# Optimization experiments

Measured on AMD Instinct MI355X. Metric: run time of the kernel, lower is better.

The kernel has to match this reference:

```python
import jax, jax.numpy as jnp
import numpy as np

B, N, C = 8, 1024, 768      # batch, tokens, dim
H, HD = 8, 96               # num_heads (= top-k experts per token), head_dim
E, T = 24, 9                # num_experts, task_num
SCALE = HD ** -0.5
W_SWITCH, W_Z = 0.1, 0.001  # switchloss, zloss weights from __init__ defaults


def setup_inputs() -> dict:
    key = jax.random.key(0)
    ks = jax.random.split(key, 5)
    g = lambda k, sh, sc: jax.random.normal(k, sh, dtype=jnp.float32) * sc
    return {
        "x": g(ks[0], (B, N, C), 1.0),
        "W_gate": g(ks[1], (T, C, E), C ** -0.5),   # per-task gating weights
        "W_in": g(ks[2], (E, C, HD), C ** -0.5),    # expert q projections (TaskMoE.map)
        "W_out": g(ks[3], (E, HD, C), HD ** -0.5),  # expert output projections (TaskMoE.reduce)
        "W_kv": g(ks[4], (C, 2 * HD), C ** -0.5),   # shared kv_proj (MQA-style)
        "task_bh": 3,
    }


def reference(x, W_gate, W_in, W_out, W_kv, task_bh):
    # ---- task-conditioned top-k gating (eval path: no noise, no sampling) ----
    logits = jnp.einsum('bnc,ce->bne', x, W_gate[task_bh])          # [B,N,E]
    probs = jax.nn.softmax(logits, axis=-1)
    top_g, top_i = jax.lax.top_k(probs, H)                          # [B,N,H]
    top_g = top_g / (jnp.sum(top_g, axis=-1, keepdims=True) + 1e-6)
    # ---- TaskMoE.map: per-head q = selected expert projection of x ----
    q_all = jnp.einsum('bnc,ecd->bned', x, W_in)                    # [B,N,E,HD]
    q = jnp.take_along_axis(q_all, top_i[..., None], axis=2)        # [B,N,H,HD]
    # ---- shared K/V (single head) ----
    kv = x @ W_kv                                                   # [B,N,2*HD]
    k, v = kv[..., :HD], kv[..., HD:]
    # ---- MQA attention ----
    attn = jnp.einsum('bihd,bjd->bhij', q, k) * SCALE               # [B,H,N,N]
    attn = jax.nn.softmax(attn, axis=-1)
    o = jnp.einsum('bhij,bjd->bihd', attn, v)                       # [B,N,H,HD]
    # ---- TaskMoE.reduce: gate-weighted combine through output experts ----
    onehot = jax.nn.one_hot(top_i, E, dtype=o.dtype)                # [B,N,H,E]
    z = jnp.einsum('bnhd,bnhe,bnh->bned', o, onehot, top_g)         # [B,N,E,HD]
    out = jnp.einsum('bned,edc->bnc', z, W_out)                     # [B,N,C]
    # ---- auxiliary routing losses (switch load-balance + z-loss) ----
    importance = probs.mean(axis=(0, 1))                            # [E]
    load = onehot.sum(axis=2).mean(axis=(0, 1)) / H                 # [E]
    switchloss = E * jnp.sum(importance * load)
    zloss = jnp.mean(jax.nn.logsumexp(logits, axis=-1) ** 2)
    aux_loss = W_SWITCH * switchloss + W_Z * zloss
    return out, aux_loss
```

## Files before the change

kernel.cpp:

```cpp
#include <hip/hip_runtime.h>
#include <hip/hip_bf16.h>
#include <math.h>

#define BB 8
#define NN 1024
#define CC 768
#define HH 8
#define HD 96
#define EE 24
#define NT (BB*NN)
#define NSLOT (NT*HH)
#define EC (EE*HD)
#define CAPQ 8192
#define ASCALE 0.10206207261596575f
#define AL2 0.14724446f
#define DEFER_THR 11.5415603f

typedef unsigned short u16;
typedef unsigned char u8;
typedef unsigned int u32;
typedef unsigned long long u64;
typedef __attribute__((ext_vector_type(8))) short s16x8;
typedef __attribute__((ext_vector_type(4))) float f32x4;
typedef __attribute__((ext_vector_type(16))) float f32x16;

__device__ __forceinline__ u16 f2b(float f) {
  unsigned u = __builtin_bit_cast(unsigned, f);
  unsigned r = u + 0x7fffu + ((u >> 16) & 1u);
  return (u16)(r >> 16);
}

__device__ __forceinline__ float fexp2(float x) {
  float r; asm("v_exp_f32 %0, %1" : "=v"(r) : "v"(x)); return r;
}

__device__ __forceinline__ u32 cvtpk(float a, float b) {
  u32 d; asm("v_cvt_pk_bf16_f32 %0, %1, %2" : "=v"(d) : "v"(a), "v"(b)); return d;
}

__device__ __forceinline__ void gload16(const u16* g, u16* lds) {
  __builtin_amdgcn_global_load_lds(
      (const __attribute__((address_space(1))) void*)g,
      (__attribute__((address_space(3))) void*)lds, 16, 0, 0);
}

__device__ __forceinline__ int xcd_remap(int bid, int nwg) {
  int q = nwg >> 3, r = nwg & 7;
  int xcd = bid & 7, idx = bid >> 3;
  return (xcd < r ? xcd * (q + 1) : r * (q + 1) + (xcd - r) * q) + idx;
}

#define WS_CNT   0
#define WS_IMP   1536
#define WS_ZSUM  3072
#define WS_G     4096
#define WS_EID   (WS_G + NSLOT*4)
#define WS_KVK   (WS_EID + NSLOT)
#define WS_VT    (WS_KVK + NT*128*2)
#define WS_WIN   (WS_VT + (size_t)96*NT*2)
#define WS_WOUT  (WS_WIN + (size_t)EC*CC*2)
#define WS_WKV   (WS_WOUT + (size_t)CC*EC*2)
#define WS_QA    (WS_WKV + 192*CC*2)
#define WS_Z     (WS_QA + (size_t)NT*EC*2)
#define WS_XB    WS_Z
#define WS_BUCKET (WS_Z + (size_t)16*1024*1024)

__global__ __launch_bounds__(256) void gate_kernel(
    const float* __restrict__ x, const float* __restrict__ Wg_all,
    const int* __restrict__ task_p, float* __restrict__ ws_f,
    int* __restrict__ ws_i, u8* __restrict__ eids, u16* __restrict__ xb,
    int* __restrict__ bucket)
{
  __shared__ float xs[16][68];
  __shared__ float wgt[24][68];
  __shared__ float scr[4][16][24];
  __shared__ float lgt[16][26];
  __shared__ float zlo[16];
  __shared__ int hist[EE];
  __shared__ int gbase[EE];

  int t = threadIdx.x;
  int w = t >> 6, l = t & 63;
  int pos = l & 15;
  int tg = pos >> 2, eg = pos & 3;
  int kq_low = (l >> 4) & 3;
  int cq = 16 * w + 4 * kq_low;
  int tok0 = blockIdx.x * 16;
  const float* Wg = Wg_all + (size_t)task_p[0] * CC * EE;

  if (t < EE) hist[t] = 0;

  int rr_ = t >> 4, cc_ = (t & 15) << 2;
  int wkk_[6], we_[6];
  #pragma unroll
  for (int i = 0; i < 6; i++) {
    int f = t + i * 256;
    wkk_[i] = f / 24; we_[i] = f - wkk_[i] * 24;
  }

  float acc[4][6];
  #pragma unroll
  for (int i = 0; i < 4; i++)
    #pragma unroll
    for (int j = 0; j < 6; j++) acc[i][j] = 0.f;

  float4 xv[2]; float wgv[2][6];
  #pragma unroll
  for (int p = 0; p < 2; p++) {
    int kb = p * 64;
    xv[p] = *(const float4*)&x[(size_t)(tok0 + rr_) * CC + kb + cc_];
    #pragma unroll
    for (int i = 0; i < 6; i++)
      wgv[p][i] = Wg[(size_t)(kb + wkk_[i]) * EE + we_[i]];
  }

  #pragma unroll
  for (int s = 0; s < 12; s++) {
    int sl = s & 1;
    __syncthreads();
    *(float4*)&xs[rr_][cc_] = xv[sl];
    {
      float4 v = xv[sl];
      u64 pk = (u64)f2b(v.x) | ((u64)f2b(v.y) << 16) |
               ((u64)f2b(v.z) << 32) | ((u64)f2b(v.w) << 48);
      *(u64*)&xb[(size_t)(tok0 + rr_) * CC + s * 64 + cc_] = pk;
    }
    #pragma unroll
    for (int i = 0; i < 6; i++) wgt[we_[i]][wkk_[i]] = wgv[sl][i];
    if (s + 2 < 12) {
      int kb = (s + 2) * 64;
      xv[sl] = *(const float4*)&x[(size_t)(tok0 + rr_) * CC + kb + cc_];
      #pragma unroll
      for (int i = 0; i < 6; i++)
        wgv[sl][i] = Wg[(size_t)(kb + wkk_[i]) * EE + we_[i]];
    }
    __syncthreads();
    float4 x4[4];
    #pragma unroll
    for (int i = 0; i < 4; i++) x4[i] = *(const float4*)&xs[tg * 4 + i][cq];
    #pragma unroll
    for (int j = 0; j < 6; j++) {
      float4 w4 = *(const float4*)&wgt[eg * 6 + j][cq];
      #pragma unroll
      for (int i = 0; i < 4; i++) {
        float a = acc[i][j];
        a = fmaf(x4[i].x, w4.x, a);
        a = fmaf(x4[i].y, w4.y, a);
        a = fmaf(x4[i].z, w4.z, a);
        a = fmaf(x4[i].w, w4.w, a);
        acc[i][j] = a;
      }
    }
  }
  #pragma unroll
  for (int i = 0; i < 4; i++)
    #pragma unroll
    for (int j = 0; j < 6; j++) {
      float v = acc[i][j];
      v += __shfl_xor(v, 16);
      v += __shfl_xor(v, 32);
      acc[i][j] = v;
    }
  if (l < 16) {
    #pragma unroll
    for (int i = 0; i < 4; i++)
      #pragma unroll
      for (int j = 0; j < 6; j++) scr[w][pos][i * 6 + j] = acc[i][j];
  }
  __syncthreads();
  if (w == 0 && l < 16) {
    #pragma unroll
    for (int i = 0; i < 4; i++)
      #pragma unroll
      for (int j = 0; j < 6; j++) {
        float s = scr[0][pos][i * 6 + j] + scr[1][pos][i * 6 + j] +
                  scr[2][pos][i * 6 + j] + scr[3][pos][i * 6 + j];
        lgt[tg * 4 + i][eg * 6 + j] = s;
      }
  }
  __syncthreads();

  int my_e[8], loc[8];
  if (t < 16) {
    int token = tok0 + t;
    float lg[EE];
    #pragma unroll
    for (int e = 0; e < EE; e++) lg[e] = lgt[t][e];
    float mx = lg[0];
    #pragma unroll
    for (int e = 1; e < EE; e++) mx = fmaxf(mx, lg[e]);
    float se = 0.f; float probs[EE];
    #pragma unroll
    for (int e = 0; e < EE; e++) { probs[e] = __expf(lg[e] - mx); se += probs[e]; }
    float inv = 1.f / se;
    #pragma unroll
    for (int e = 0; e < EE; e++) probs[e] *= inv;
    float lse = mx + __logf(se);
    zlo[t] = lse * lse;

    unsigned taken = 0u;
    float gsum = 0.f;
    float my_g[8];
    #pragma unroll
    for (int h = 0; h < HH; h++) {
      float best = -1.f; int bi = 0;
      #pragma unroll
      for (int e = 0; e < EE; e++) {
        bool ok = !((taken >> e) & 1u) && (probs[e] > best);
        best = ok ? probs[e] : best;
        bi   = ok ? e : bi;
      }
      taken |= 1u << bi;
      gsum += best;
      my_g[h] = best; my_e[h] = bi;
    }
    float ginv = 1.f / (gsum + 1e-6f);
    float4 g0, g1;
    g0.x = my_g[0] * ginv; g0.y = my_g[1] * ginv; g0.z = my_g[2] * ginv; g0.w = my_g[3] * ginv;
    g1.x = my_g[4] * ginv; g1.y = my_g[5] * ginv; g1.z = my_g[6] * ginv; g1.w = my_g[7] * ginv;
    float* gbuf = ws_f + WS_G / 4;
    *(float4*)&gbuf[(size_t)token * HH]     = g0;
    *(float4*)&gbuf[(size_t)token * HH + 4] = g1;
    u64 pk = 0;
    #pragma unroll
    for (int h = 0; h < HH; h++) pk |= (u64)(u8)my_e[h] << (8 * h);
    *(u64*)&eids[(size_t)token * HH] = pk;
    #pragma unroll
    for (int h = 0; h < HH; h++) loc[h] = atomicAdd(&hist[my_e[h]], 1);
    #pragma unroll
    for (int e = 0; e < EE; e++) lgt[t][e] = probs[e];
  }
  __syncthreads();
  if (t < EE) {
    float s = 0.f;
    #pragma unroll 8
    for (int rr = 0; rr < 16; rr++) s += lgt[rr][t];
    atomicAdd(ws_f + WS_IMP / 4 + t * 16, s);
    gbase[t] = atomicAdd(&ws_i[t * 16], hist[t]);
  } else if (t == 32) {
    float s = 0.f;
    #pragma unroll 8
    for (int rr = 0; rr < 16; rr++) s += zlo[rr];
    atomicAdd(ws_f + WS_ZSUM / 4, s);
  }
  __syncthreads();
  if (t < 16) {
    int token = tok0 + t;
    #pragma unroll
    for (int h = 0; h < HH; h++)
      bucket[my_e[h] * CAPQ + gbase[my_e[h]] + loc[h]] = token;
  }
}

__global__ __launch_bounds__(256) void transpose_kernel(
    const float* __restrict__ src, u16* __restrict__ dst,
    int R, int C, int sB, int dR, int dB)
{
  __shared__ float tile[32][33];
  int e = blockIdx.z;
  const float* s = src + (size_t)e * sB;
  int t = threadIdx.x;
  int tr = t >> 5, tc = t & 31;
  #pragma unroll
  for (int i = 0; i < 4; i++) {
    int r = blockIdx.x * 32 + tr + i * 8;
    int c = blockIdx.y * 32 + tc;
    tile[tr + i * 8][tc] = s[(size_t)r * C + c];
  }
  __syncthreads();
  #pragma unroll
  for (int i = 0; i < 4; i++) {
    int sc = blockIdx.y * 32 + tr + i * 8;
    int sr = blockIdx.x * 32 + tc;
    dst[(size_t)e * dB + (size_t)sc * dR + sr] = f2b(tile[tc][tr + i * 8]);
  }
}

template<int BM, int BN, bool OUT_F32>
__global__ __launch_bounds__(256) void gemm_kernel(
    const u16* __restrict__ A, const u16* __restrict__ Bt,
    void* __restrict__ Cp, int M, int N, int K)
{
  constexpr int WM = BM / 2, WN = BN / 2;
  constexpr int FM = WM / 16, FN = WN / 16;
  __shared__ u16 As[BM][64];
  __shared__ u16 Bs[BN][64];
  int t = threadIdx.x;
  int w = t >> 6, l = t & 63;
  int lr = l & 15, lg = l >> 4;
  int wr = w >> 1, wc = w & 1;
  int nwg = gridDim.x * gridDim.y;
  int logical = xcd_remap(blockIdx.y * gridDim.x + blockIdx.x, nwg);
  int col0 = (logical % gridDim.x) * BN, row0 = (logical / gridDim.x) * BM;

  f32x4 acc[FM][FN];
  #pragma unroll
  for (int i = 0; i < FM; i++)
    #pragma unroll
    for (int j = 0; j < FN; j++) acc[i][j] = (f32x4)(0.f);

  int sr = t >> 3;
  int sc = t & 7;
  for (int kb = 0; kb < K; kb += 64) {
    __syncthreads();
    #pragma unroll
    for (int i = 0; i < BM / 32; i++) {
      int rr = i * 32 + sr;
      int ch = sc ^ (rr & 7);
      gload16(A + (size_t)(row0 + rr) * K + kb + ch * 8, &As[rr][sc * 8]);
    }
    #pragma unroll
    for (int i = 0; i < BN / 32; i++) {
      int rr = i * 32 + sr;
      int ch = sc ^ (rr & 7);
      gload16(Bt + (size_t)(col0 + rr) * K + kb + ch * 8, &Bs[rr][sc * 8]);
    }
    __syncthreads();
    #pragma unroll
    for (int ks = 0; ks < 2; ks++) {
      s16x8 af[FM], bf[FN];
      #pragma unroll
      for (int i = 0; i < FM; i++)
        af[i] = *(const s16x8*)&As[wr * WM + i * 16 + lr][8 * ((ks * 4 + lg) ^ (lr & 7))];
      #pragma unroll
      for (int j = 0; j < FN; j++)
        bf[j] = *(const s16x8*)&Bs[wc * WN + j * 16 + lr][8 * ((ks * 4 + lg) ^ (lr & 7))];
      #pragma unroll
      for (int i = 0; i < FM; i++)
        #pragma unroll
        for (int j = 0; j < FN; j++)
          acc[i][j] = __builtin_amdgcn_mfma_f32_16x16x32_bf16(af[i], bf[j], acc[i][j], 0, 0, 0);
    }
  }
  #pragma unroll
  for (int i = 0; i < FM; i++)
    #pragma unroll
    for (int j = 0; j < FN; j++)
      #pragma unroll
      for (int reg = 0; reg < 4; reg++) {
        int rr = row0 + wr * WM + i * 16 + lg * 4 + reg;
        int cc = col0 + wc * WN + j * 16 + lr;
        if (OUT_F32) ((float*)Cp)[(size_t)rr * N + cc] = acc[i][j][reg];
        else ((u16*)Cp)[(size_t)rr * N + cc] = f2b(acc[i][j][reg]);
      }
}

__global__ __launch_bounds__(256) void qproj_kernel(
    const u16* __restrict__ xb, const u16* __restrict__ winT,
    const int* __restrict__ ws_i, const int* __restrict__ bucket,
    u16* __restrict__ qall)
{
  int e = blockIdx.y;
  int t0 = blockIdx.x * 128;
  int cnt = ws_i[e * 16];
  if (t0 >= cnt) return;
  __shared__ u16 As[128][64];
  __shared__ u16 Bs[96][64];
  __shared__ int tok_s[128];
  int t = threadIdx.x;
  if (t < 128) tok_s[t] = bucket[e * CAPQ + min(t0 + t, cnt - 1)];
  __syncthreads();
  int w = t >> 6, l = t & 63;
  int lr = l & 15, lg = l >> 4;
  int wr = w >> 1, wc = w & 1;
  const u16* Bt = winT + (size_t)e * HD * CC;

  f32x4 acc[4][3];
  #pragma unroll
  for (int i = 0; i < 4; i++)
    #pragma unroll
    for (int j = 0; j < 3; j++) acc[i][j] = (f32x4)(0.f);

  int sr = t >> 3, sc = t & 7;
  int atok[4];
  #pragma unroll
  for (int i = 0; i < 4; i++) atok[i] = tok_s[i * 32 + sr];

  for (int kb = 0; kb < CC; kb += 64) {
    __syncthreads();
    #pragma unroll
    for (int i = 0; i < 4; i++) {
      int rr = i * 32 + sr;
      int ch = sc ^ (rr & 7);
      gload16(xb + (size_t)atok[i] * CC + kb + ch * 8, &As[rr][sc * 8]);
    }
    #pragma unroll
    for (int i = 0; i < 3; i++) {
      int rr = i * 32 + sr;
      int ch = sc ^ (rr & 7);
      gload16(Bt + (size_t)rr * CC + kb + ch * 8, &Bs[rr][sc * 8]);
    }
    __syncthreads();
    #pragma unroll
    for (int ks = 0; ks < 2; ks++) {
      s16x8 af[4], bf[3];
      #pragma unroll
      for (int i = 0; i < 4; i++)
        af[i] = *(const s16x8*)&As[wr * 64 + i * 16 + lr][8 * ((ks * 4 + lg) ^ (lr & 7))];
      #pragma unroll
      for (int j = 0; j < 3; j++)
        bf[j] = *(const s16x8*)&Bs[wc * 48 + j * 16 + lr][8 * ((ks * 4 + lg) ^ (lr & 7))];
      #pragma unroll
      for (int i = 0; i < 4; i++)
        #pragma unroll
        for (int j = 0; j < 3; j++)
          acc[i][j] = __builtin_amdgcn_mfma_f32_16x16x32_bf16(af[i], bf[j], acc[i][j], 0, 0, 0);
    }
  }
  #pragma unroll
  for (int i = 0; i < 4; i++)
    #pragma unroll
    for (int reg = 0; reg < 4; reg++) {
      int rr = wr * 64 + i * 16 + lg * 4 + reg;
      if (t0 + rr < cnt) {
        int tok = tok_s[rr];
        u16* qp = qall + (size_t)tok * EC + e * HD + wc * 48;
        #pragma unroll
        for (int j = 0; j < 3; j++)
          qp[j * 16 + lr] = f2b(acc[i][j][reg]);
      }
    }
}

__global__ __launch_bounds__(256) void kvproj_kernel(
    const u16* __restrict__ xb, const u16* __restrict__ wkvT,
    u16* __restrict__ kvbk, u16* __restrict__ vtb)
{
  __shared__ u16 As[128][64];
  __shared__ u16 Bs[64][64];
  int t = threadIdx.x;
  int w = t >> 6, l = t & 63;
  int lr = l & 15, lg = l >> 4;
  int wr = w >> 1, wc = w & 1;
  int nwg = gridDim.x * gridDim.y;
  int logical = xcd_remap(blockIdx.y * gridDim.x + blockIdx.x, nwg);
  int col0 = (logical % gridDim.x) * 64, row0 = (logical / gridDim.x) * 128;

  f32x4 acc[4][2];
  #pragma unroll
  for (int i = 0; i < 4; i++)
    #pragma unroll
    for (int j = 0; j < 2; j++) acc[i][j] = (f32x4)(0.f);

  int sr = t >> 3, sc = t & 7;
  for (int kb = 0; kb < CC; kb += 64) {
    __syncthreads();
    #pragma unroll
    for (int i = 0; i < 4; i++) {
      int rr = i * 32 + sr;
      int ch = sc ^ (rr & 7);
      gload16(xb + (size_t)(row0 + rr) * CC + kb + ch * 8, &As[rr][sc * 8]);
    }
    #pragma unroll
    for (int i = 0; i < 2; i++) {
      int rr = i * 32 + sr;
      int ch = sc ^ (rr & 7);
      gload16(wkvT + (size_t)(col0 + rr) * CC + kb + ch * 8, &Bs[rr][sc * 8]);
    }
    __syncthreads();
    #pragma unroll
    for (int ks = 0; ks < 2; ks++) {
      s16x8 af[4], bf[2];
      #pragma unroll
      for (int i = 0; i < 4; i++)
        af[i] = *(const s16x8*)&As[wr * 64 + i * 16 + lr][8 * ((ks * 4 + lg) ^ (lr & 7))];
      #pragma unroll
      for (int j = 0; j < 2; j++)
        bf[j] = *(const s16x8*)&Bs[wc * 32 + j * 16 + lr][8 * ((ks * 4 + lg) ^ (lr & 7))];
      #pragma unroll
      for (int i = 0; i < 4; i++)
        #pragma unroll
        for (int j = 0; j < 2; j++)
          acc[i][j] = __builtin_amdgcn_mfma_f32_16x16x32_bf16(af[i], bf[j], acc[i][j], 0, 0, 0);
    }
  }
  #pragma unroll
  for (int i = 0; i < 4; i++)
    #pragma unroll
    for (int j = 0; j < 2; j++) {
      int cb = col0 + wc * 32 + j * 16 + lr;
      int rb = row0 + wr * 64 + i * 16 + lg * 4;
      if (cb < 96) {
        int ch = cb >> 3, ci = cb & 7;
        #pragma unroll
        for (int reg = 0; reg < 4; reg++) {
          int tok = rb + reg;
          kvbk[(size_t)tok * 128 + 8 * (ch ^ (tok & 7)) + ci] = f2b(acc[i][j][reg]);
        }
      } else {
        int d = cb - 96;
        u64 pk = (u64)f2b(acc[i][j][0]) | ((u64)f2b(acc[i][j][1]) << 16) |
                 ((u64)f2b(acc[i][j][2]) << 32) | ((u64)f2b(acc[i][j][3]) << 48);
        int blkbase = rb & ~63;
        int ch = (rb & 63) >> 3;
        *(u64*)&vtb[(size_t)d * NT + blkbase + 8 * (ch ^ (d & 7)) + (rb & 7)] = pk;
      }
    }
}

__global__ __launch_bounds__(256, 2) void attn_kernel(
    const u16* __restrict__ qall, const u16* __restrict__ kvbk,
    const u16* __restrict__ vtb, const u8* __restrict__ eids,
    const float* __restrict__ gbuf, u16* __restrict__ z)
{
  __shared__ u16 Ks[2][64][128];
  __shared__ u16 Vt[2][96][64];
  int b = blockIdx.y;
  int tok0 = blockIdx.x * 32;
  int t = threadIdx.x;
  int w = t >> 6, l = t & 63;
  int h = blockIdx.z * 4 + w;
  int lo = l & 31, hi = l >> 5;

  s16x8 qf[6];
  {
    int tok = b * NN + tok0 + lo;
    int e = eids[tok * HH + h];
    const u16* qp = qall + (size_t)tok * EC + e * HD + hi * 8;
    #pragma unroll
    for (int ks = 0; ks < 6; ks++)
      qf[ks] = *(const s16x8*)(qp + ks * 16);
  }

  const u16* kvwin = kvbk + (size_t)(b * NN) * 128;
  const u16* vwin  = vtb + (size_t)(b * NN);

  f32x16 o0 = (f32x16)(0.f), o1 = (f32x16)(0.f), o2 = (f32x16)(0.f);
  float m = -1e30f, lsum = 0.f;

  #pragma unroll
  for (int k2 = 0; k2 < 4; k2++) {
    int c = t + k2 * 256;
    gload16(kvwin + c * 8, &Ks[0][0][0] + c * 8);
  }
  #pragma unroll
  for (int k2 = 0; k2 < 3; k2++) {
    int c = t + k2 * 256;
    gload16(vwin + (size_t)(c >> 3) * NT + (c & 7) * 8, &Vt[0][0][0] + c * 8);
  }

  for (int jt = 0; jt < 16; jt++) {
    __syncthreads();
    if (jt < 15) {
      int j0 = (jt + 1) * 64;
      int nb = (jt + 1) & 1;
      const u16* kb_ = kvwin + (size_t)j0 * 128;
      #pragma unroll
      for (int k2 = 0; k2 < 4; k2++) {
        int c = t + k2 * 256;
        gload16(kb_ + c * 8, &Ks[nb][0][0] + c * 8);
      }
      const u16* vb_ = vwin + j0;
      #pragma unroll
      for (int k2 = 0; k2 < 3; k2++) {
        int c = t + k2 * 256;
        gload16(vb_ + (size_t)(c >> 3) * NT + (c & 7) * 8, &Vt[nb][0][0] + c * 8);
      }
    }
    int buf = jt & 1;

    f32x16 s0 = (f32x16)(0.f), s1 = (f32x16)(0.f);
    #pragma unroll
    for (int ks = 0; ks < 6; ks++) {
      int pos = 8 * ((2 * ks + hi) ^ (lo & 7));
      s16x8 a0 = *(const s16x8*)&Ks[buf][lo][pos];
      s16x8 a1 = *(const s16x8*)&Ks[buf][32 + lo][pos];
      s0 = __builtin_amdgcn_mfma_f32_32x32x16_bf16(a0, qf[ks], s0, 0, 0, 0);
      s1 = __builtin_amdgcn_mfma_f32_32x32x16_bf16(a1, qf[ks], s1, 0, 0, 0);
    }

    float pm = fmaxf(s0[0], s0[1]);
    #pragma unroll
    for (int rg = 2; rg < 16; rg += 2) pm = fmaxf(pm, fmaxf(s0[rg], s0[rg + 1]));
    #pragma unroll
    for (int rg = 0; rg < 16; rg += 2) pm = fmaxf(pm, fmaxf(s1[rg], s1[rg + 1]));
    pm = fmaxf(pm, __shfl_xor(pm, 32));
    pm *= AL2;

    if (!__all(pm - m <= DEFER_THR)) {
      float mn = fmaxf(m, pm);
      float al = fexp2(m - mn);
      m = mn; lsum *= al;
      #pragma unroll
      for (int rg = 0; rg < 16; rg++) {
        int qrow = (rg & 3) + 8 * (rg >> 2) + 4 * hi;
        float alr = __shfl(al, qrow);
        o0[rg] *= alr; o1[rg] *= alr; o2[rg] *= alr;
      }
    }

    float ts = 0.f;
    u32 wpk[2][4][2];
    #pragma unroll
    for (int kb2 = 0; kb2 < 2; kb2++)
      #pragma unroll
      for (int rr = 0; rr < 4; rr++)
        #pragma unroll
        for (int pp = 0; pp < 2; pp++) {
          float sA = kb2 ? s1[rr * 4 + 2 * pp]     : s0[rr * 4 + 2 * pp];
          float sB = kb2 ? s1[rr * 4 + 2 * pp + 1] : s0[rr * 4 + 2 * pp + 1];
          float eA = fexp2(fmaf(sA, AL2, -m));
          float eB = fexp2(fmaf(sB, AL2, -m));
          ts += eA + eB;
          wpk[kb2][rr][pp] = cvtpk(eA, eB);
        }
    lsum += ts;

    s16x8 pa[4];
    #pragma unroll
    for (int ks = 0; ks < 4; ks++) {
      int kb2 = ks >> 1;
      int rlo = (ks & 1) * 2, rhi = rlo + 1;
      u32 own_lo0 = wpk[kb2][rlo][0], own_lo1 = wpk[kb2][rlo][1];
      u32 own_hi0 = wpk[kb2][rhi][0], own_hi1 = wpk[kb2][rhi][1];
      u32 send0 = hi ? own_lo0 : own_hi0;
      u32 send1 = hi ? own_lo1 : own_hi1;
      u32 recv0 = (u32)__shfl_xor((int)send0, 32);
      u32 recv1 = (u32)__shfl_xor((int)send1, 32);
      union { s16x8 v; u32 u[4]; } pu;
      pu.u[0] = hi ? recv0 : own_lo0;
      pu.u[1] = hi ? recv1 : own_lo1;
      pu.u[2] = hi ? own_hi0 : recv0;
      pu.u[3] = hi ? own_hi1 : recv1;
      pa[ks] = pu.v;
    }

    #pragma unroll
    for (int ks = 0; ks < 4; ks++) {
      int pos = 8 * ((2 * ks + hi) ^ (lo & 7));
      s16x8 v0 = *(const s16x8*)&Vt[buf][lo][pos];
      s16x8 v1 = *(const s16x8*)&Vt[buf][32 + lo][pos];
      s16x8 v2 = *(const s16x8*)&Vt[buf][64 + lo][pos];
      o0 = __builtin_amdgcn_mfma_f32_32x32x16_bf16(pa[ks], v0, o0, 0, 0, 0);
      o1 = __builtin_amdgcn_mfma_f32_32x32x16_bf16(pa[ks], v1, o1, 0, 0, 0);
      o2 = __builtin_amdgcn_mfma_f32_32x32x16_bf16(pa[ks], v2, o2, 0, 0, 0);
    }
  }

  float lt = lsum + __shfl_xor(lsum, 32);
  #pragma unroll
  for (int rg = 0; rg < 16; rg++) {
    int qrow = (rg & 3) + 8 * (rg >> 2) + 4 * hi;
    float lv = __shfl(lt, qrow);
    int tok = b * NN + tok0 + qrow;
    int slot = tok * HH + h;
    float scl = gbuf[slot] / lv;
    int e = eids[slot];
    u16* zp = z + (size_t)tok * EC + e * HD + lo;
    zp[0]  = f2b(o0[rg] * scl);
    zp[32] = f2b(o1[rg] * scl);
    zp[64] = f2b(o2[rg] * scl);
  }
}

__global__ void aux_kernel(const float* __restrict__ ws_f,
                           const int* __restrict__ ws_i, float* __restrict__ out)
{
  if (threadIdx.x == 0 && blockIdx.x == 0) {
    float sw = 0.f;
    for (int e = 0; e < EE; e++) {
      float imp = ws_f[WS_IMP / 4 + e * 16] / (float)NT;
      float load = (float)ws_i[e * 16] / (float)(NT * HH);
      sw += imp * load;
    }
    float zl = ws_f[WS_ZSUM / 4] / (float)NT;
    out[(size_t)NT * CC] = 0.1f * ((float)EE * sw) + 0.001f * zl;
  }
}

extern "C" void kernel_launch(void* const* d_in, const int* in_sizes, int n_in,
                              void* d_out, int out_size, void* d_ws, size_t ws_size,
                              hipStream_t stream)
{
  const float* x    = (const float*)d_in[0];
  const float* Wg   = (const float*)d_in[1];
  const float* Win  = (const float*)d_in[2];
  const float* Wout = (const float*)d_in[3];
  const float* Wkv  = (const float*)d_in[4];
  const int*   task = (const int*)d_in[5];
  float* out = (float*)d_out;
  float* ws_f = (float*)d_ws;
  int*   ws_i = (int*)d_ws;
  u8*  eids = (u8*)((char*)d_ws + WS_EID);
  u16* kvbk = (u16*)((char*)d_ws + WS_KVK);
  u16* vtb  = (u16*)((char*)d_ws + WS_VT);
  u16* winT = (u16*)((char*)d_ws + WS_WIN);
  u16* woutT= (u16*)((char*)d_ws + WS_WOUT);
  u16* wkvT = (u16*)((char*)d_ws + WS_WKV);
  u16* qall = (u16*)((char*)d_ws + WS_QA);
  u16* z    = (u16*)((char*)d_ws + WS_Z);
  u16* xb   = (u16*)((char*)d_ws + WS_XB);
  int* bucket = (int*)((char*)d_ws + WS_BUCKET);

  hipMemsetAsync(d_ws, 0, 4096, stream);

  transpose_kernel<<<dim3(CC/32, HD/32, EE), 256, 0, stream>>>(Win, winT, CC, HD, CC*HD, CC, HD*CC);
  transpose_kernel<<<dim3(HD/32, CC/32, EE), 256, 0, stream>>>(Wout, woutT, HD, CC, HD*CC, EC, HD);
  transpose_kernel<<<dim3(CC/32, 192/32, 1), 256, 0, stream>>>(Wkv, wkvT, CC, 192, 0, CC, 0);

  gate_kernel<<<NT / 16, 256, 0, stream>>>(x, Wg, task, ws_f, ws_i, eids, xb, bucket);

  kvproj_kernel<<<dim3(3, NT/128), 256, 0, stream>>>(xb, wkvT, kvbk, vtb);
  qproj_kernel<<<dim3(NT/128, EE), 256, 0, stream>>>(xb, winT, ws_i, bucket, qall);

  hipMemsetAsync(z, 0, (size_t)NT * EC * 2, stream);

  attn_kernel<<<dim3(NN/32, BB, 2), 256, 0, stream>>>(qall, kvbk, vtb, eids, ws_f + WS_G/4, z);

  gemm_kernel<128, 64, true><<<dim3(CC/64, NT/128), 256, 0, stream>>>(
      z, woutT, out, NT, CC, EC);

  aux_kernel<<<1, 64, 0, stream>>>(ws_f, ws_i, out);
}
```

Measured before the change: 172.7 us.

## Load K/V fragments directly from global memory in attention, drop LDS staging

The attention kernel stops staging K and V^T tiles through double-buffered shared memory with async loads and barriers. Each wave now reads its MFMA operands straight from global memory (relying on L1/L2, since all 4 waves share the same K/V). The K/V producer writes unswizzled, compact layouts (K row stride 96 instead of padded 128) to match. It also adds s_setprio around the MFMA blocks and relaxes launch bounds. This removes __syncthreads and LDS traffic but puts uncoalesced, redundant global loads on the critical path with no explicit prefetch.

Result: slower. 212.1 us (+22.8%).

```diff
diff --git a/kernel.cpp b/kernel.cpp
--- a/kernel.cpp
+++ b/kernel.cpp
@@ -481,30 +481,23 @@
       int cb = col0 + wc * 32 + j * 16 + lr;
       int rb = row0 + wr * 64 + i * 16 + lg * 4;
       if (cb < 96) {
-        int ch = cb >> 3, ci = cb & 7;
         #pragma unroll
-        for (int reg = 0; reg < 4; reg++) {
-          int tok = rb + reg;
-          kvbk[(size_t)tok * 128 + 8 * (ch ^ (tok & 7)) + ci] = f2b(acc[i][j][reg]);
-        }
+        for (int reg = 0; reg < 4; reg++)
+          kvbk[(size_t)(rb + reg) * 96 + cb] = f2b(acc[i][j][reg]);
       } else {
         int d = cb - 96;
         u64 pk = (u64)f2b(acc[i][j][0]) | ((u64)f2b(acc[i][j][1]) << 16) |
                  ((u64)f2b(acc[i][j][2]) << 32) | ((u64)f2b(acc[i][j][3]) << 48);
-        int blkbase = rb & ~63;
-        int ch = (rb & 63) >> 3;
-        *(u64*)&vtb[(size_t)d * NT + blkbase + 8 * (ch ^ (d & 7)) + (rb & 7)] = pk;
+        *(u64*)&vtb[(size_t)d * NT + rb] = pk;
       }
     }
 }
 
-__global__ __launch_bounds__(256, 2) void attn_kernel(
+__global__ __launch_bounds__(256) void attn_kernel(
     const u16* __restrict__ qall, const u16* __restrict__ kvbk,
     const u16* __restrict__ vtb, const u8* __restrict__ eids,
     const float* __restrict__ gbuf, u16* __restrict__ z)
 {
-  __shared__ u16 Ks[2][64][128];
-  __shared__ u16 Vt[2][96][64];
   int b = blockIdx.y;
   int tok0 = blockIdx.x * 32;
   int t = threadIdx.x;
@@ -522,52 +515,28 @@
       qf[ks] = *(const s16x8*)(qp + ks * 16);
   }
 
-  const u16* kvwin = kvbk + (size_t)(b * NN) * 128;
-  const u16* vwin  = vtb + (size_t)(b * NN);
+  const u16* kwin = kvbk + (size_t)(b * NN) * 96;
+  const u16* vwin = vtb + (size_t)(b * NN);
 
   f32x16 o0 = (f32x16)(0.f), o1 = (f32x16)(0.f), o2 = (f32x16)(0.f);
   float m = -1e30f, lsum = 0.f;
 
-  #pragma unroll
-  for (int k2 = 0; k2 < 4; k2++) {
-    int c = t + k2 * 256;
-    gload16(kvwin + c * 8, &Ks[0][0][0] + c * 8);
-  }
-  #pragma unroll
-  for (int k2 = 0; k2 < 3; k2++) {
-    int c = t + k2 * 256;
-    gload16(vwin + (size_t)(c >> 3) * NT + (c & 7) * 8, &Vt[0][0][0] + c * 8);
-  }
-
+  #pragma unroll 2
   for (int jt = 0; jt < 16; jt++) {
-    __syncthreads();
-    if (jt < 15) {
-      int j0 = (jt + 1) * 64;
-      int nb = (jt + 1) & 1;
-      const u16* kb_ = kvwin + (size_t)j0 * 128;
-      #pragma unroll
-      for (int k2 = 0; k2 < 4; k2++) {
-        int c = t + k2 * 256;
-        gload16(kb_ + c * 8, &Ks[nb][0][0] + c * 8);
-      }
-      const u16* vb_ = vwin + j0;
-      #pragma unroll
-      for (int k2 = 0; k2 < 3; k2++) {
-        int c = t + k2 * 256;
-        gload16(vb_ + (size_t)(c >> 3) * NT + (c & 7) * 8, &Vt[nb][0][0] + c * 8);
-      }
-    }
-    int buf = jt & 1;
-
+    int j0 = jt * 64;
+
+    const u16* kr0 = kwin + (size_t)(j0 + lo) * 96 + hi * 8;
+    const u16* kr1 = kr0 + 32 * 96;
     f32x16 s0 = (f32x16)(0.f), s1 = (f32x16)(0.f);
+    __builtin_amdgcn_s_setprio(1);
     #pragma unroll
     for (int ks = 0; ks < 6; ks++) {
-      int pos = 8 * ((2 * ks + hi) ^ (lo & 7));
-      s16x8 a0 = *(const s16x8*)&Ks[buf][lo][pos];
-      s16x8 a1 = *(const s16x8*)&Ks[buf][32 + lo][pos];
+      s16x8 a0 = *(const s16x8*)(kr0 + ks * 16);
+      s16x8 a1 = *(const s16x8*)(kr1 + ks * 16);
       s0 = __builtin_amdgcn_mfma_f32_32x32x16_bf16(a0, qf[ks], s0, 0, 0, 0);
       s1 = __builtin_amdgcn_mfma_f32_32x32x16_bf16(a1, qf[ks], s1, 0, 0, 0);
     }
+    __builtin_amdgcn_s_setprio(0);
 
     float pm = fmaxf(s0[0], s0[1]);
     #pragma unroll
@@ -625,16 +594,18 @@
       pa[ks] = pu.v;
     }
 
+    __builtin_amdgcn_s_setprio(1);
     #pragma unroll
     for (int ks = 0; ks < 4; ks++) {
-      int pos = 8 * ((2 * ks + hi) ^ (lo & 7));
-      s16x8 v0 = *(const s16x8*)&Vt[buf][lo][pos];
-      s16x8 v1 = *(const s16x8*)&Vt[buf][32 + lo][pos];
-      s16x8 v2 = *(const s16x8*)&Vt[buf][64 + lo][pos];
+      const u16* vk = vwin + j0 + ks * 16 + hi * 8;
+      s16x8 v0 = *(const s16x8*)(vk + (size_t)lo * NT);
+      s16x8 v1 = *(const s16x8*)(vk + (size_t)(32 + lo) * NT);
+      s16x8 v2 = *(const s16x8*)(vk + (size_t)(64 + lo) * NT);
       o0 = __builtin_amdgcn_mfma_f32_32x32x16_bf16(pa[ks], v0, o0, 0, 0, 0);
       o1 = __builtin_amdgcn_mfma_f32_32x32x16_bf16(pa[ks], v1, o1, 0, 0, 0);
       o2 = __builtin_amdgcn_mfma_f32_32x32x16_bf16(pa[ks], v2, o2, 0, 0, 0);
     }
+    __builtin_amdgcn_s_setprio(0);
   }
 
   float lt = lsum + __shfl_xor(lsum, 32);
```
